# Performance work log

Hardware: AMD Instinct MI355X
Metric: run time of the kernel (lower is better)

The kernel has to match this reference:

```python
import jax, jax.numpy as jnp
import numpy as np

N_VEH = 40000
N_PATH = 400000
N_ACTOR = 128
N_MAP = 128
ACT_C = 32
PAT_C = 32
SIZE = N_ACTOR + N_MAP + ACT_C + PAT_C  # 320
HID = SIZE // 2  # 160
EPS = 1e-5


def _gn1(x, w, b):
    # GroupNorm with 1 group over channel dim of [N, C]: per-row normalize, per-channel affine
    mu = jnp.mean(x, axis=-1, keepdims=True)
    var = jnp.mean(jnp.square(x - mu), axis=-1, keepdims=True)
    return (x - mu) * jax.lax.rsqrt(var + EPS) * w + b


def setup_inputs() -> dict:
    key = jax.random.key(0)
    ks = jax.random.split(key, 12)
    inp = {
        "actors": jax.random.normal(ks[0], (N_VEH, N_ACTOR), jnp.float32),
        "paths": jax.random.normal(ks[1], (N_PATH, N_MAP), jnp.float32),
        "Z_act": jax.random.normal(ks[2], (N_VEH, ACT_C), jnp.float32),
        "Z_pat": jax.random.normal(ks[3], (N_PATH, PAT_C), jnp.float32),
        "u": jax.random.randint(ks[4], (N_PATH,), 0, N_VEH, jnp.int64 if jax.config.jax_enable_x64 else jnp.int32),
        # LinRes params (LaneGCN LinearRes: Linear(bias=False) -> GN -> ReLU -> Linear(bias=False) -> GN -> +transform(x) -> ReLU)
        "w1": jax.random.normal(ks[5], (HID, SIZE), jnp.float32) / np.sqrt(SIZE),
        "w2": jax.random.normal(ks[6], (HID, HID), jnp.float32) / np.sqrt(HID),
        "wt": jax.random.normal(ks[7], (HID, SIZE), jnp.float32) / np.sqrt(SIZE),
        "g1w": jnp.ones((HID,), jnp.float32),
        "g1b": jnp.zeros((HID,), jnp.float32),
        "g2w": jnp.ones((HID,), jnp.float32),
        "g2b": jnp.zeros((HID,), jnp.float32),
        # final head Linear(HID, 1)
        "wh": jax.random.normal(ks[8], (1, HID), jnp.float32) / np.sqrt(HID),
        "bh": jnp.zeros((1,), jnp.float32),
    }
    return inp


def reference(actors, paths, Z_act, Z_pat, u, w1, w2, wt, g1w, g1b, g2w, g2b, wh, bh):
    # edge-indexed gather + concat: [N_PATH, SIZE]
    x = jnp.concatenate([paths, Z_pat, actors[u], Z_act[u]], axis=-1)
    h = jnp.einsum('ns,hs->nh', x, w1)
    h = jax.nn.relu(_gn1(h, g1w, g1b))
    h = jnp.einsum('nh,gh->ng', h, w2)
    h = _gn1(h, g2w, g2b)
    h = jax.nn.relu(h + jnp.einsum('ns,hs->nh', x, wt))
    logits = jnp.einsum('nh,oh->no', h, wh) + bh
    return logits
```

## Files before the change

### kernel.cpp

```cpp
#include <hip/hip_runtime.h>
#include <hip/hip_bf16.h>

typedef short short8 __attribute__((ext_vector_type(8)));
typedef float floatx4 __attribute__((ext_vector_type(4)));

#define XP 328
#define HP 168

__device__ __forceinline__ unsigned short f2bf(float f) {
    __hip_bfloat16 h = __float2bfloat16(f);
    return __builtin_bit_cast(unsigned short, h);
}
__device__ __forceinline__ float bf2f(unsigned short s) {
    __hip_bfloat16 h = __builtin_bit_cast(__hip_bfloat16, s);
    return __bfloat162float(h);
}

__device__ __forceinline__ float dpp_sum16(float v) {
    v += __builtin_bit_cast(float, __builtin_amdgcn_update_dpp(
             0, __builtin_bit_cast(int, v), 0x128, 0xF, 0xF, true));
    v += __builtin_bit_cast(float, __builtin_amdgcn_update_dpp(
             0, __builtin_bit_cast(int, v), 0x124, 0xF, 0xF, true));
    v += __builtin_bit_cast(float, __builtin_amdgcn_update_dpp(
             0, __builtin_bit_cast(int, v), 0x122, 0xF, 0xF, true));
    v += __builtin_bit_cast(float, __builtin_amdgcn_update_dpp(
             0, __builtin_bit_cast(int, v), 0x121, 0xF, 0xF, true));
    return v;
}

__global__ void pack_wc(const float* __restrict__ w1, const float* __restrict__ wt,
                        unsigned short* __restrict__ dst) {
    int i = blockIdx.x * 256 + threadIdx.x;
    if (i >= 320 * 320) return;
    int j = i & 7;
    int lane = (i >> 3) & 63;
    int r = i >> 9;
    int kb = r % 10;
    int t = r / 10;
    int n = t * 16 + (lane & 15);
    int k = kb * 32 + ((lane >> 4) << 3) + j;
    float v = (n < 160) ? w1[n * 320 + k] : wt[(n - 160) * 320 + k];
    dst[i] = f2bf(v);
}

__global__ void pack_w2(const float* __restrict__ w2, unsigned short* __restrict__ dst) {
    int i = blockIdx.x * 256 + threadIdx.x;
    if (i >= 160 * 160) return;
    int j = i & 7;
    int lane = (i >> 3) & 63;
    int r = i >> 9;
    int kb = r % 5;
    int t = r / 5;
    int n = t * 16 + (lane & 15);
    int k = kb * 32 + ((lane >> 4) << 3) + j;
    dst[i] = f2bf(w2[n * 160 + k]);
}

__global__ __launch_bounds__(256, 3) void fused_kernel(
    const float* __restrict__ actors, const float* __restrict__ paths,
    const float* __restrict__ Z_act, const float* __restrict__ Z_pat,
    const int* __restrict__ u,
    const unsigned short* __restrict__ pB1, const unsigned short* __restrict__ pB2,
    const float* __restrict__ g1w, const float* __restrict__ g1b,
    const float* __restrict__ g2w, const float* __restrict__ g2b,
    const float* __restrict__ wh, const float* __restrict__ bh,
    float* __restrict__ out)
{
    __shared__ __align__(16) char smem[43520];
    unsigned short* lX  = (unsigned short*)smem;
    unsigned short* lH1 = (unsigned short*)smem;
    unsigned short* lHT = (unsigned short*)(smem + 21504);
    float*  sSum  = (float*)(smem + 41984);
    float*  sSq   = sSum + 128;
    float2* sStat = (float2*)(smem + 41984 + 1024);

    const int tid  = threadIdx.x;
    const int wave = tid >> 6;
    const int lane = tid & 63;
    const int quad = lane >> 4;
    const int l15  = lane & 15;
    const int row0 = blockIdx.x * 64;

    float4 vD[10], vG[10];
    int uv[10];
    #pragma unroll
    for (int i = 0; i < 10; i++) {
        int f = i * 256 + tid;
        int r = f / 40, q = f - r * 40;
        const float* src = (q < 32) ? (paths + (size_t)(row0 + r) * 128 + q * 4)
                                    : (Z_pat + (size_t)(row0 + r) * 32 + (q - 32) * 4);
        vD[i] = *(const float4*)src;
        uv[i] = u[row0 + r];
    }
    #pragma unroll
    for (int i = 0; i < 10; i++) {
        int f = i * 256 + tid;
        int r = f / 40, q = f - r * 40;
        (void)r;
        int un = uv[i];
        const float* src = (q < 32) ? (actors + (size_t)un * 128 + q * 4)
                                    : (Z_act + (size_t)un * 32 + (q - 32) * 4);
        vG[i] = *(const float4*)src;
    }
    #pragma unroll
    for (int i = 0; i < 10; i++) {
        int f = i * 256 + tid;
        int r = f / 40, q = f - r * 40;
        ushort4 sv;
        sv.x = f2bf(vD[i].x); sv.y = f2bf(vD[i].y); sv.z = f2bf(vD[i].z); sv.w = f2bf(vD[i].w);
        *(ushort4*)(lX + r * XP + q * 4) = sv;
    }
    #pragma unroll
    for (int i = 0; i < 10; i++) {
        int f = i * 256 + tid;
        int r = f / 40, q = f - r * 40;
        ushort4 sv;
        sv.x = f2bf(vG[i].x); sv.y = f2bf(vG[i].y); sv.z = f2bf(vG[i].z); sv.w = f2bf(vG[i].w);
        *(ushort4*)(lX + r * XP + 160 + q * 4) = sv;
    }

    short8 bA[5], bB[5];
    #pragma unroll
    for (int ti = 0; ti < 5; ti++) {
        int t = wave * 5 + ti;
        bA[ti] = *(const short8*)(pB1 + ((size_t)(t * 10 + 0) * 64 + lane) * 8);
        bB[ti] = *(const short8*)(pB1 + ((size_t)(t * 10 + 1) * 64 + lane) * 8);
    }
    __syncthreads();

    floatx4 fzero = {0.f, 0.f, 0.f, 0.f};
    floatx4 acc[4][5];
    #pragma unroll
    for (int i = 0; i < 4; i++)
        #pragma unroll
        for (int j = 0; j < 5; j++) acc[i][j] = fzero;

    #pragma unroll
    for (int kb = 0; kb < 10; kb++) {
        short8 a[4];
        #pragma unroll
        for (int mt = 0; mt < 4; mt++)
            a[mt] = *(const short8*)(lX + (mt * 16 + l15) * XP + kb * 32 + quad * 8);
        short8 bN[5];
        if (kb + 2 < 10) {
            #pragma unroll
            for (int ti = 0; ti < 5; ti++) {
                int t = wave * 5 + ti;
                bN[ti] = *(const short8*)(pB1 + ((size_t)(t * 10 + kb + 2) * 64 + lane) * 8);
            }
        }
        #pragma unroll
        for (int ti = 0; ti < 5; ti++) {
            #pragma unroll
            for (int mt = 0; mt < 4; mt++)
                acc[mt][ti] = __builtin_amdgcn_mfma_f32_16x16x32_bf16(a[mt], bA[ti], acc[mt][ti], 0, 0, 0);
        }
        #pragma unroll
        for (int ti = 0; ti < 5; ti++) { bA[ti] = bB[ti]; bB[ti] = bN[ti]; }
    }
    __syncthreads();

    if (wave >= 2) {
        int wn2 = wave - 2;
        #pragma unroll
        for (int mtp = 0; mtp < 4; mtp++)
            #pragma unroll
            for (int ti = 0; ti < 5; ti++) {
                ushort4 sv;
                sv.x = f2bf(acc[mtp][ti][0]);
                sv.y = f2bf(acc[mtp][ti][1]);
                sv.z = f2bf(acc[mtp][ti][2]);
                sv.w = f2bf(acc[mtp][ti][3]);
                int ch = wn2 * 80 + ti * 16 + l15;
                int rg = (mtp * 4 + quad) ^ l15;
                *(ushort4*)(lHT + ch * 64 + rg * 4) = sv;
            }
    } else {
        float s[16], q2[16];
        #pragma unroll
        for (int mt = 0; mt < 4; mt++)
            #pragma unroll
            for (int r = 0; r < 4; r++) {
                float sv = 0.f, qv = 0.f;
                #pragma unroll
                for (int ti = 0; ti < 5; ti++) {
                    float v = acc[mt][ti][r];
                    sv += v; qv += v * v;
                }
                s[mt * 4 + r] = sv; q2[mt * 4 + r] = qv;
            }
        #pragma unroll
        for (int k = 0; k < 16; k++) {
            s[k]  = dpp_sum16(s[k]);
            q2[k] = dpp_sum16(q2[k]);
        }
        if (l15 == 0) {
            #pragma unroll
            for (int mt = 0; mt < 4; mt++)
                #pragma unroll
                for (int r = 0; r < 4; r++) {
                    int m = mt * 16 + quad * 4 + r;
                    sSum[wave * 64 + m] = s[mt * 4 + r];
                    sSq[wave * 64 + m]  = q2[mt * 4 + r];
                }
        }
    }
    __syncthreads();

    if (tid < 64) {
        float ts = sSum[tid] + sSum[64 + tid];
        float tq = sSq[tid] + sSq[64 + tid];
        float mu = ts * (1.f / 160.f);
        float var = tq * (1.f / 160.f) - mu * mu;
        float2 st; st.x = mu; st.y = rsqrtf(var + 1e-5f);
        sStat[tid] = st;
    }
    __syncthreads();

    if (wave < 2) {
        float gw[5], gb[5];
        #pragma unroll
        for (int ti = 0; ti < 5; ti++) {
            int n = wave * 80 + ti * 16 + l15;
            gw[ti] = g1w[n]; gb[ti] = g1b[n];
        }
        #pragma unroll
        for (int mt = 0; mt < 4; mt++)
            #pragma unroll
            for (int r = 0; r < 4; r++) {
                int m = mt * 16 + quad * 4 + r;
                float2 st = sStat[m];
                #pragma unroll
                for (int ti = 0; ti < 5; ti++) {
                    float v = (acc[mt][ti][r] - st.x) * st.y * gw[ti] + gb[ti];
                    v = fmaxf(v, 0.f);
                    lH1[m * HP + wave * 80 + ti * 16 + l15] = f2bf(v);
                }
            }
    }

    const int wm = wave & 1, wn = wave >> 1;
    short8 b2A[5], b2B[5];
    #pragma unroll
    for (int ti = 0; ti < 5; ti++) {
        int t = wn * 5 + ti;
        b2A[ti] = *(const short8*)(pB2 + ((size_t)(t * 5 + 0) * 64 + lane) * 8);
        b2B[ti] = *(const short8*)(pB2 + ((size_t)(t * 5 + 1) * 64 + lane) * 8);
    }
    __syncthreads();

    floatx4 acc2[2][5];
    #pragma unroll
    for (int i = 0; i < 2; i++)
        #pragma unroll
        for (int j = 0; j < 5; j++) acc2[i][j] = fzero;

    #pragma unroll
    for (int kb = 0; kb < 5; kb++) {
        short8 a[2];
        #pragma unroll
        for (int mt = 0; mt < 2; mt++)
            a[mt] = *(const short8*)(lH1 + (wm * 32 + mt * 16 + l15) * HP + kb * 32 + quad * 8);
        short8 bN[5];
        if (kb + 2 < 5) {
            #pragma unroll
            for (int ti = 0; ti < 5; ti++) {
                int t = wn * 5 + ti;
                bN[ti] = *(const short8*)(pB2 + ((size_t)(t * 5 + kb + 2) * 64 + lane) * 8);
            }
        }
        #pragma unroll
        for (int ti = 0; ti < 5; ti++) {
            #pragma unroll
            for (int mt = 0; mt < 2; mt++)
                acc2[mt][ti] = __builtin_amdgcn_mfma_f32_16x16x32_bf16(a[mt], b2A[ti], acc2[mt][ti], 0, 0, 0);
        }
        #pragma unroll
        for (int ti = 0; ti < 5; ti++) { b2A[ti] = b2B[ti]; b2B[ti] = bN[ti]; }
    }

    {
        float s[8], q2[8];
        #pragma unroll
        for (int mt = 0; mt < 2; mt++)
            #pragma unroll
            for (int r = 0; r < 4; r++) {
                float sv = 0.f, qv = 0.f;
                #pragma unroll
                for (int ti = 0; ti < 5; ti++) {
                    float v = acc2[mt][ti][r];
                    sv += v; qv += v * v;
                }
                s[mt * 4 + r] = sv; q2[mt * 4 + r] = qv;
            }
        #pragma unroll
        for (int k = 0; k < 8; k++) {
            s[k]  = dpp_sum16(s[k]);
            q2[k] = dpp_sum16(q2[k]);
        }
        if (l15 == 0) {
            #pragma unroll
            for (int mt = 0; mt < 2; mt++)
                #pragma unroll
                for (int r = 0; r < 4; r++) {
                    int m = wm * 32 + mt * 16 + quad * 4 + r;
                    sSum[wn * 64 + m] = s[mt * 4 + r];
                    sSq[wn * 64 + m]  = q2[mt * 4 + r];
                }
        }
    }
    __syncthreads();

    if (tid < 64) {
        float ts = sSum[tid] + sSum[64 + tid];
        float tq = sSq[tid] + sSq[64 + tid];
        float mu = ts * (1.f / 160.f);
        float var = tq * (1.f / 160.f) - mu * mu;
        float2 st; st.x = mu; st.y = rsqrtf(var + 1e-5f);
        sStat[tid] = st;
    }
    __syncthreads();

    {
        float g2wv[5], g2bv[5], whv[5];
        #pragma unroll
        for (int ti = 0; ti < 5; ti++) {
            int n = wn * 80 + ti * 16 + l15;
            g2wv[ti] = g2w[n]; g2bv[ti] = g2b[n]; whv[ti] = wh[n];
        }
        float2 st2[2][4];
        #pragma unroll
        for (int mt = 0; mt < 2; mt++)
            #pragma unroll
            for (int r = 0; r < 4; r++)
                st2[mt][r] = sStat[wm * 32 + mt * 16 + quad * 4 + r];

        float dp[8];
        #pragma unroll
        for (int k = 0; k < 8; k++) dp[k] = 0.f;

        #pragma unroll
        for (int mt = 0; mt < 2; mt++)
            #pragma unroll
            for (int ti = 0; ti < 5; ti++) {
                int ch = wn * 80 + ti * 16 + l15;
                int rg = ((wm * 2 + mt) * 4 + quad) ^ l15;
                ushort4 hv = *(const ushort4*)(lHT + ch * 64 + rg * 4);
                float hvf[4];
                hvf[0] = bf2f(hv.x); hvf[1] = bf2f(hv.y);
                hvf[2] = bf2f(hv.z); hvf[3] = bf2f(hv.w);
                #pragma unroll
                for (int r = 0; r < 4; r++) {
                    float v = (acc2[mt][ti][r] - st2[mt][r].x) * st2[mt][r].y * g2wv[ti] + g2bv[ti];
                    v += hvf[r];
                    v = fmaxf(v, 0.f);
                    dp[mt * 4 + r] += v * whv[ti];
                }
            }
        #pragma unroll
        for (int k = 0; k < 8; k++) dp[k] = dpp_sum16(dp[k]);
        if (l15 == 0) {
            #pragma unroll
            for (int mt = 0; mt < 2; mt++)
                #pragma unroll
                for (int r = 0; r < 4; r++) {
                    int m = wm * 32 + mt * 16 + quad * 4 + r;
                    sSum[wn * 64 + m] = dp[mt * 4 + r];
                }
        }
    }
    __syncthreads();
    if (tid < 64) out[row0 + tid] = sSum[tid] + sSum[64 + tid] + bh[0];
}

extern "C" void kernel_launch(void* const* d_in, const int* in_sizes, int n_in,
                              void* d_out, int out_size, void* d_ws, size_t ws_size,
                              hipStream_t stream) {
    const float* actors = (const float*)d_in[0];
    const float* paths  = (const float*)d_in[1];
    const float* Z_act  = (const float*)d_in[2];
    const float* Z_pat  = (const float*)d_in[3];
    const int*   u      = (const int*)d_in[4];
    const float* w1     = (const float*)d_in[5];
    const float* w2     = (const float*)d_in[6];
    const float* wt     = (const float*)d_in[7];
    const float* g1w    = (const float*)d_in[8];
    const float* g1b    = (const float*)d_in[9];
    const float* g2w    = (const float*)d_in[10];
    const float* g2b    = (const float*)d_in[11];
    const float* wh     = (const float*)d_in[12];
    const float* bh     = (const float*)d_in[13];
    float* out = (float*)d_out;

    unsigned short* pB1 = (unsigned short*)d_ws;
    unsigned short* pB2 = pB1 + 320 * 320;

    hipLaunchKernelGGL(pack_wc, dim3(400), dim3(256), 0, stream, w1, wt, pB1);
    hipLaunchKernelGGL(pack_w2, dim3(100), dim3(256), 0, stream, w2, pB2);
    hipLaunchKernelGGL(fused_kernel, dim3(400000 / 64), dim3(256), 0, stream,
                       actors, paths, Z_act, Z_pat, u, pB1, pB2,
                       g1w, g1b, g2w, g2b, wh, bh, out);
}
```

Baseline: 486.0 us.

## Shrink blocks to 32 rows with 2 waves, swizzled LDS A layout and weight ring

Blocks now process 32 rows with 128 threads. Each wave owns a whole 160-channel output half: wave 0 takes the W1 half and wave 1 the transform half. This lets wave 0 compute the first GroupNorm stats entirely in registers, and lets wave 1 keep its transform outputs in registers instead of writing them to LDS. The input tile is stored in LDS in an MFMA-fragment-packed, XOR-swizzled layout so A-operand reads avoid bank conflicts, and the B-operand weights stream through a 5-deep register ring. The changes cut shared memory and barriers and raise occupancy, at the cost of each wave re-reading the full weight matrix for fewer rows, which means more weight traffic per row.

```diff
diff --git a/kernel.cpp b/kernel.cpp
--- a/kernel.cpp
+++ b/kernel.cpp
@@ -2,9 +2,9 @@
 #include <hip/hip_bf16.h>
 
 typedef short short8 __attribute__((ext_vector_type(8)));
+typedef unsigned short ushortv8 __attribute__((ext_vector_type(8)));
 typedef float floatx4 __attribute__((ext_vector_type(4)));
 
-#define XP 328
 #define HP 168
 
 __device__ __forceinline__ unsigned short f2bf(float f) {
@@ -56,7 +56,7 @@
     dst[i] = f2bf(w2[n * 160 + k]);
 }
 
-__global__ __launch_bounds__(256, 3) void fused_kernel(
+__global__ __launch_bounds__(128, 4) void fused_kernel(
     const float* __restrict__ actors, const float* __restrict__ paths,
     const float* __restrict__ Z_act, const float* __restrict__ Z_pat,
     const int* __restrict__ u,
@@ -66,292 +66,250 @@
     const float* __restrict__ wh, const float* __restrict__ bh,
     float* __restrict__ out)
 {
-    __shared__ __align__(16) char smem[43520];
+    __shared__ __align__(16) char smem[20480];
     unsigned short* lX  = (unsigned short*)smem;
     unsigned short* lH1 = (unsigned short*)smem;
-    unsigned short* lHT = (unsigned short*)(smem + 21504);
-    float*  sSum  = (float*)(smem + 41984);
-    float*  sSq   = sSum + 128;
-    float2* sStat = (float2*)(smem + 41984 + 1024);
+    unsigned short* lHT = (unsigned short*)(smem + 10752);
+    float* sP  = (float*)(smem + 15872);
+    float* sDp = (float*)(smem + 16384);
 
     const int tid  = threadIdx.x;
     const int wave = tid >> 6;
     const int lane = tid & 63;
     const int quad = lane >> 4;
     const int l15  = lane & 15;
-    const int row0 = blockIdx.x * 64;
-
-    float4 vD[10], vG[10];
-    int uv[10];
-    #pragma unroll
-    for (int i = 0; i < 10; i++) {
-        int f = i * 256 + tid;
-        int r = f / 40, q = f - r * 40;
-        const float* src = (q < 32) ? (paths + (size_t)(row0 + r) * 128 + q * 4)
-                                    : (Z_pat + (size_t)(row0 + r) * 32 + (q - 32) * 4);
-        vD[i] = *(const float4*)src;
+    const int row0 = blockIdx.x * 32;
+
+    float4 vD[5][2], vG[5][2];
+    int uv[5], rr[5], qq[5];
+    #pragma unroll
+    for (int i = 0; i < 5; i++) {
+        int f = i * 128 + tid;
+        int r = f / 20, q = f - r * 20;
+        rr[i] = r; qq[i] = q;
+        const float* src = (q < 16) ? (paths + (size_t)(row0 + r) * 128 + q * 8)
+                                    : (Z_pat + (size_t)(row0 + r) * 32 + (q - 16) * 8);
+        vD[i][0] = *(const float4*)src;
+        vD[i][1] = *(const float4*)(src + 4);
         uv[i] = u[row0 + r];
     }
     #pragma unroll
-    for (int i = 0; i < 10; i++) {
-        int f = i * 256 + tid;
-        int r = f / 40, q = f - r * 40;
-        (void)r;
+    for (int i = 0; i < 5; i++) {
+        int q = qq[i];
         int un = uv[i];
-        const float* src = (q < 32) ? (actors + (size_t)un * 128 + q * 4)
-                                    : (Z_act + (size_t)un * 32 + (q - 32) * 4);
-        vG[i] = *(const float4*)src;
-    }
-    #pragma unroll
-    for (int i = 0; i < 10; i++) {
-        int f = i * 256 + tid;
-        int r = f / 40, q = f - r * 40;
-        ushort4 sv;
-        sv.x = f2bf(vD[i].x); sv.y = f2bf(vD[i].y); sv.z = f2bf(vD[i].z); sv.w = f2bf(vD[i].w);
-        *(ushort4*)(lX + r * XP + q * 4) = sv;
-    }
-    #pragma unroll
-    for (int i = 0; i < 10; i++) {
-        int f = i * 256 + tid;
-        int r = f / 40, q = f - r * 40;
-        ushort4 sv;
-        sv.x = f2bf(vG[i].x); sv.y = f2bf(vG[i].y); sv.z = f2bf(vG[i].z); sv.w = f2bf(vG[i].w);
-        *(ushort4*)(lX + r * XP + 160 + q * 4) = sv;
-    }
-
-    short8 bA[5], bB[5];
-    #pragma unroll
-    for (int ti = 0; ti < 5; ti++) {
-        int t = wave * 5 + ti;
-        bA[ti] = *(const short8*)(pB1 + ((size_t)(t * 10 + 0) * 64 + lane) * 8);
-        bB[ti] = *(const short8*)(pB1 + ((size_t)(t * 10 + 1) * 64 + lane) * 8);
+        const float* src = (q < 16) ? (actors + (size_t)un * 128 + q * 8)
+                                    : (Z_act + (size_t)un * 32 + (q - 16) * 8);
+        vG[i][0] = *(const float4*)src;
+        vG[i][1] = *(const float4*)(src + 4);
+    }
+    #pragma unroll
+    for (int i = 0; i < 5; i++) {
+        int r = rr[i], q = qq[i];
+        int mt = r >> 4;
+        {
+            int kb = q >> 2, qd = q & 3;
+            int slot = ((r & 15) | (qd << 4)) ^ ((qd ^ kb) & 7);
+            ushortv8 sv;
+            sv[0] = f2bf(vD[i][0].x); sv[1] = f2bf(vD[i][0].y);
+            sv[2] = f2bf(vD[i][0].z); sv[3] = f2bf(vD[i][0].w);
+            sv[4] = f2bf(vD[i][1].x); sv[5] = f2bf(vD[i][1].y);
+            sv[6] = f2bf(vD[i][1].z); sv[7] = f2bf(vD[i][1].w);
+            *(ushortv8*)(lX + ((mt * 10 + kb) * 64 + slot) * 8) = sv;
+        }
+        {
+            int q8 = q + 20;
+            int kb = q8 >> 2, qd = q8 & 3;
+            int slot = ((r & 15) | (qd << 4)) ^ ((qd ^ kb) & 7);
+            ushortv8 sv;
+            sv[0] = f2bf(vG[i][0].x); sv[1] = f2bf(vG[i][0].y);
+            sv[2] = f2bf(vG[i][0].z); sv[3] = f2bf(vG[i][0].w);
+            sv[4] = f2bf(vG[i][1].x); sv[5] = f2bf(vG[i][1].y);
+            sv[6] = f2bf(vG[i][1].z); sv[7] = f2bf(vG[i][1].w);
+            *(ushortv8*)(lX + ((mt * 10 + kb) * 64 + slot) * 8) = sv;
+        }
+    }
+
+    const unsigned short* pBw = pB1 + (size_t)wave * 51200 + (size_t)lane * 8;
+    short8 ring[5];
+    #pragma unroll
+    for (int p = 0; p < 5; p++) {
+        ring[p] = *(const short8*)(pBw + (size_t)(p * 10) * 512);
     }
     __syncthreads();
 
     floatx4 fzero = {0.f, 0.f, 0.f, 0.f};
-    floatx4 acc[4][5];
-    #pragma unroll
-    for (int i = 0; i < 4; i++)
-        #pragma unroll
-        for (int j = 0; j < 5; j++) acc[i][j] = fzero;
+    floatx4 acc[2][10];
+    #pragma unroll
+    for (int i = 0; i < 2; i++)
+        #pragma unroll
+        for (int j = 0; j < 10; j++) acc[i][j] = fzero;
 
     #pragma unroll
     for (int kb = 0; kb < 10; kb++) {
-        short8 a[4];
-        #pragma unroll
-        for (int mt = 0; mt < 4; mt++)
-            a[mt] = *(const short8*)(lX + (mt * 16 + l15) * XP + kb * 32 + quad * 8);
-        short8 bN[5];
-        if (kb + 2 < 10) {
-            #pragma unroll
-            for (int ti = 0; ti < 5; ti++) {
-                int t = wave * 5 + ti;
-                bN[ti] = *(const short8*)(pB1 + ((size_t)(t * 10 + kb + 2) * 64 + lane) * 8);
-            }
-        }
-        #pragma unroll
-        for (int ti = 0; ti < 5; ti++) {
-            #pragma unroll
-            for (int mt = 0; mt < 4; mt++)
-                acc[mt][ti] = __builtin_amdgcn_mfma_f32_16x16x32_bf16(a[mt], bA[ti], acc[mt][ti], 0, 0, 0);
-        }
-        #pragma unroll
-        for (int ti = 0; ti < 5; ti++) { bA[ti] = bB[ti]; bB[ti] = bN[ti]; }
-    }
-    __syncthreads();
-
-    if (wave >= 2) {
-        int wn2 = wave - 2;
-        #pragma unroll
-        for (int mtp = 0; mtp < 4; mtp++)
-            #pragma unroll
-            for (int ti = 0; ti < 5; ti++) {
-                ushort4 sv;
-                sv.x = f2bf(acc[mtp][ti][0]);
-                sv.y = f2bf(acc[mtp][ti][1]);
-                sv.z = f2bf(acc[mtp][ti][2]);
-                sv.w = f2bf(acc[mtp][ti][3]);
-                int ch = wn2 * 80 + ti * 16 + l15;
-                int rg = (mtp * 4 + quad) ^ l15;
-                *(ushort4*)(lHT + ch * 64 + rg * 4) = sv;
-            }
-    } else {
-        float s[16], q2[16];
-        #pragma unroll
-        for (int mt = 0; mt < 4; mt++)
+        int sl = (lane ^ ((quad ^ kb) & 7)) * 8;
+        short8 a0 = *(const short8*)(lX + kb * 512 + sl);
+        short8 a1 = *(const short8*)(lX + 5120 + kb * 512 + sl);
+        #pragma unroll
+        for (int ti = 0; ti < 10; ti++) {
+            int p = kb * 10 + ti;
+            short8 b = ring[p % 5];
+            acc[0][ti] = __builtin_amdgcn_mfma_f32_16x16x32_bf16(a0, b, acc[0][ti], 0, 0, 0);
+            acc[1][ti] = __builtin_amdgcn_mfma_f32_16x16x32_bf16(a1, b, acc[1][ti], 0, 0, 0);
+            if (p + 5 < 100) {
+                int p2 = p + 5, kb2 = p2 / 10, ti2 = p2 - kb2 * 10;
+                ring[p2 % 5] = *(const short8*)(pBw + (size_t)(ti2 * 10 + kb2) * 512);
+            }
+        }
+    }
+    __syncthreads();
+
+    ushort4 hk[2][5];
+    if (wave == 0) {
+        float mu_[2][4], rs_[2][4];
+        #pragma unroll
+        for (int mt = 0; mt < 2; mt++)
             #pragma unroll
             for (int r = 0; r < 4; r++) {
-                float sv = 0.f, qv = 0.f;
+                float s = 0.f, q2 = 0.f;
                 #pragma unroll
-                for (int ti = 0; ti < 5; ti++) {
+                for (int ti = 0; ti < 10; ti++) {
                     float v = acc[mt][ti][r];
-                    sv += v; qv += v * v;
-                }
-                s[mt * 4 + r] = sv; q2[mt * 4 + r] = qv;
-            }
-        #pragma unroll
-        for (int k = 0; k < 16; k++) {
-            s[k]  = dpp_sum16(s[k]);
-            q2[k] = dpp_sum16(q2[k]);
-        }
-        if (l15 == 0) {
-            #pragma unroll
-            for (int mt = 0; mt < 4; mt++)
+                    s += v; q2 += v * v;
+                }
+                s = dpp_sum16(s); q2 = dpp_sum16(q2);
+                float mu = s * (1.f / 160.f);
+                float var = q2 * (1.f / 160.f) - mu * mu;
+                mu_[mt][r] = mu;
+                rs_[mt][r] = rsqrtf(var + 1e-5f);
+            }
+        float gw[10], gb[10];
+        #pragma unroll
+        for (int ti = 0; ti < 10; ti++) {
+            int n = ti * 16 + l15;
+            gw[ti] = g1w[n]; gb[ti] = g1b[n];
+        }
+        #pragma unroll
+        for (int mt = 0; mt < 2; mt++)
+            #pragma unroll
+            for (int ti = 0; ti < 10; ti++)
                 #pragma unroll
                 for (int r = 0; r < 4; r++) {
-                    int m = mt * 16 + quad * 4 + r;
-                    sSum[wave * 64 + m] = s[mt * 4 + r];
-                    sSq[wave * 64 + m]  = q2[mt * 4 + r];
-                }
-        }
-    }
-    __syncthreads();
-
-    if (tid < 64) {
-        float ts = sSum[tid] + sSum[64 + tid];
-        float tq = sSq[tid] + sSq[64 + tid];
-        float mu = ts * (1.f / 160.f);
-        float var = tq * (1.f / 160.f) - mu * mu;
-        float2 st; st.x = mu; st.y = rsqrtf(var + 1e-5f);
-        sStat[tid] = st;
-    }
-    __syncthreads();
-
-    if (wave < 2) {
-        float gw[5], gb[5];
+                    float v = (acc[mt][ti][r] - mu_[mt][r]) * rs_[mt][r] * gw[ti] + gb[ti];
+                    v = fmaxf(v, 0.f);
+                    lH1[(mt * 16 + quad * 4 + r) * HP + ti * 16 + l15] = f2bf(v);
+                }
+    } else {
+        #pragma unroll
+        for (int mt = 0; mt < 2; mt++)
+            #pragma unroll
+            for (int tk = 0; tk < 5; tk++) {
+                ushort4 kv;
+                kv.x = f2bf(acc[mt][tk + 5][0]); kv.y = f2bf(acc[mt][tk + 5][1]);
+                kv.z = f2bf(acc[mt][tk + 5][2]); kv.w = f2bf(acc[mt][tk + 5][3]);
+                hk[mt][tk] = kv;
+                ushort4 sv;
+                sv.x = f2bf(acc[mt][tk][0]); sv.y = f2bf(acc[mt][tk][1]);
+                sv.z = f2bf(acc[mt][tk][2]); sv.w = f2bf(acc[mt][tk][3]);
+                int ch = tk * 16 + l15;
+                int rg = (mt * 4 + quad) ^ (l15 & 7);
+                *(ushort4*)(lHT + (ch * 8 + rg) * 4) = sv;
+            }
+    }
+
+    const unsigned short* pB2w = pB2 + (size_t)wave * 12800 + (size_t)lane * 8;
+    short8 ring2[4];
+    #pragma unroll
+    for (int p = 0; p < 4; p++) {
+        ring2[p] = *(const short8*)(pB2w + (size_t)(p * 5) * 512);
+    }
+    __syncthreads();
+
+    floatx4 acc2[2][5];
+    #pragma unroll
+    for (int i = 0; i < 2; i++)
+        #pragma unroll
+        for (int j = 0; j < 5; j++) acc2[i][j] = fzero;
+
+    #pragma unroll
+    for (int kb = 0; kb < 5; kb++) {
+        short8 a0 = *(const short8*)(lH1 + l15 * HP + kb * 32 + quad * 8);
+        short8 a1 = *(const short8*)(lH1 + (16 + l15) * HP + kb * 32 + quad * 8);
+        #pragma unroll
+        for (int ti = 0; ti < 5; ti++) {
+            int p = kb * 5 + ti;
+            short8 b = ring2[p % 4];
+            acc2[0][ti] = __builtin_amdgcn_mfma_f32_16x16x32_bf16(a0, b, acc2[0][ti], 0, 0, 0);
+            acc2[1][ti] = __builtin_amdgcn_mfma_f32_16x16x32_bf16(a1, b, acc2[1][ti], 0, 0, 0);
+            if (p + 4 < 25) {
+                int p2 = p + 4, kb2 = p2 / 5, ti2 = p2 - kb2 * 5;
+                ring2[p2 % 4] = *(const short8*)(pB2w + (size_t)(ti2 * 5 + kb2) * 512);
+            }
+        }
+    }
+
+    #pragma unroll
+    for (int mt = 0; mt < 2; mt++)
+        #pragma unroll
+        for (int r = 0; r < 4; r++) {
+            float s = 0.f, q2 = 0.f;
+            #pragma unroll
+            for (int ti = 0; ti < 5; ti++) {
+                float v = acc2[mt][ti][r];
+                s += v; q2 += v * v;
+            }
+            s = dpp_sum16(s); q2 = dpp_sum16(q2);
+            if (l15 == 0) {
+                int m = mt * 16 + quad * 4 + r;
+                float2 pv; pv.x = s; pv.y = q2;
+                *(float2*)(sP + m * 4 + wave * 2) = pv;
+            }
+        }
+    __syncthreads();
+
+    float mu2_[2][4], rs2_[2][4];
+    #pragma unroll
+    for (int mt = 0; mt < 2; mt++)
+        #pragma unroll
+        for (int r = 0; r < 4; r++) {
+            int m = mt * 16 + quad * 4 + r;
+            float4 pv = *(const float4*)(sP + m * 4);
+            float ts = pv.x + pv.z;
+            float tq = pv.y + pv.w;
+            float mu = ts * (1.f / 160.f);
+            float var = tq * (1.f / 160.f) - mu * mu;
+            mu2_[mt][r] = mu;
+            rs2_[mt][r] = rsqrtf(var + 1e-5f);
+        }
+
+    {
+        float g2wv[5], g2bv[5], whv[5];
         #pragma unroll
         for (int ti = 0; ti < 5; ti++) {
             int n = wave * 80 + ti * 16 + l15;
-            gw[ti] = g1w[n]; gb[ti] = g1b[n];
-        }
-        #pragma unroll
-        for (int mt = 0; mt < 4; mt++)
-            #pragma unroll
-            for (int r = 0; r < 4; r++) {
-                int m = mt * 16 + quad * 4 + r;
-                float2 st = sStat[m];
-                #pragma unroll
-                for (int ti = 0; ti < 5; ti++) {
-                    float v = (acc[mt][ti][r] - st.x) * st.y * gw[ti] + gb[ti];
-                    v = fmaxf(v, 0.f);
-                    lH1[m * HP + wave * 80 + ti * 16 + l15] = f2bf(v);
-                }
-            }
-    }
-
-    const int wm = wave & 1, wn = wave >> 1;
-    short8 b2A[5], b2B[5];
-    #pragma unroll
-    for (int ti = 0; ti < 5; ti++) {
-        int t = wn * 5 + ti;
-        b2A[ti] = *(const short8*)(pB2 + ((size_t)(t * 5 + 0) * 64 + lane) * 8);
-        b2B[ti] = *(const short8*)(pB2 + ((size_t)(t * 5 + 1) * 64 + lane) * 8);
-    }
-    __syncthreads();
-
-    floatx4 acc2[2][5];
-    #pragma unroll
-    for (int i = 0; i < 2; i++)
-        #pragma unroll
-        for (int j = 0; j < 5; j++) acc2[i][j] = fzero;
-
-    #pragma unroll
-    for (int kb = 0; kb < 5; kb++) {
-        short8 a[2];
+            g2wv[ti] = g2w[n]; g2bv[ti] = g2b[n]; whv[ti] = wh[n];
+        }
+        float dp[8];
+        #pragma unroll
+        for (int k = 0; k < 8; k++) dp[k] = 0.f;
+
         #pragma unroll
         for (int mt = 0; mt < 2; mt++)
-            a[mt] = *(const short8*)(lH1 + (wm * 32 + mt * 16 + l15) * HP + kb * 32 + quad * 8);
-        short8 bN[5];
-        if (kb + 2 < 5) {
             #pragma unroll
             for (int ti = 0; ti < 5; ti++) {
-                int t = wn * 5 + ti;
-                bN[ti] = *(const short8*)(pB2 + ((size_t)(t * 5 + kb + 2) * 64 + lane) * 8);
-            }
-        }
-        #pragma unroll
-        for (int ti = 0; ti < 5; ti++) {
-            #pragma unroll
-            for (int mt = 0; mt < 2; mt++)
-                acc2[mt][ti] = __builtin_amdgcn_mfma_f32_16x16x32_bf16(a[mt], b2A[ti], acc2[mt][ti], 0, 0, 0);
-        }
-        #pragma unroll
-        for (int ti = 0; ti < 5; ti++) { b2A[ti] = b2B[ti]; b2B[ti] = bN[ti]; }
-    }
-
-    {
-        float s[8], q2[8];
-        #pragma unroll
-        for (int mt = 0; mt < 2; mt++)
-            #pragma unroll
-            for (int r = 0; r < 4; r++) {
-                float sv = 0.f, qv = 0.f;
-                #pragma unroll
-                for (int ti = 0; ti < 5; ti++) {
-                    float v = acc2[mt][ti][r];
-                    sv += v; qv += v * v;
-                }
-                s[mt * 4 + r] = sv; q2[mt * 4 + r] = qv;
-            }
-        #pragma unroll
-        for (int k = 0; k < 8; k++) {
-            s[k]  = dpp_sum16(s[k]);
-            q2[k] = dpp_sum16(q2[k]);
-        }
-        if (l15 == 0) {
-            #pragma unroll
-            for (int mt = 0; mt < 2; mt++)
-                #pragma unroll
-                for (int r = 0; r < 4; r++) {
-                    int m = wm * 32 + mt * 16 + quad * 4 + r;
-                    sSum[wn * 64 + m] = s[mt * 4 + r];
-                    sSq[wn * 64 + m]  = q2[mt * 4 + r];
-                }
-        }
-    }
-    __syncthreads();
-
-    if (tid < 64) {
-        float ts = sSum[tid] + sSum[64 + tid];
-        float tq = sSq[tid] + sSq[64 + tid];
-        float mu = ts * (1.f / 160.f);
-        float var = tq * (1.f / 160.f) - mu * mu;
-        float2 st; st.x = mu; st.y = rsqrtf(var + 1e-5f);
-        sStat[tid] = st;
-    }
-    __syncthreads();
-
-    {
-        float g2wv[5], g2bv[5], whv[5];
-        #pragma unroll
-        for (int ti = 0; ti < 5; ti++) {
-            int n = wn * 80 + ti * 16 + l15;
-            g2wv[ti] = g2w[n]; g2bv[ti] = g2b[n]; whv[ti] = wh[n];
-        }
-        float2 st2[2][4];
-        #pragma unroll
-        for (int mt = 0; mt < 2; mt++)
-            #pragma unroll
-            for (int r = 0; r < 4; r++)
-                st2[mt][r] = sStat[wm * 32 + mt * 16 + quad * 4 + r];
-
-        float dp[8];
-        #pragma unroll
-        for (int k = 0; k < 8; k++) dp[k] = 0.f;
-
-        #pragma unroll
-        for (int mt = 0; mt < 2; mt++)
-            #pragma unroll
-            for (int ti = 0; ti < 5; ti++) {
-                int ch = wn * 80 + ti * 16 + l15;
-                int rg = ((wm * 2 + mt) * 4 + quad) ^ l15;
-                ushort4 hv = *(const ushort4*)(lHT + ch * 64 + rg * 4);
+                ushort4 hv;
+                if (wave == 0) {
+                    int ch = ti * 16 + l15;
+                    int rg = (mt * 4 + quad) ^ (l15 & 7);
+                    hv = *(const ushort4*)(lHT + (ch * 8 + rg) * 4);
+                } else {
+                    hv = hk[mt][ti];
+                }
                 float hvf[4];
                 hvf[0] = bf2f(hv.x); hvf[1] = bf2f(hv.y);
                 hvf[2] = bf2f(hv.z); hvf[3] = bf2f(hv.w);
                 #pragma unroll
                 for (int r = 0; r < 4; r++) {
-                    float v = (acc2[mt][ti][r] - st2[mt][r].x) * st2[mt][r].y * g2wv[ti] + g2bv[ti];
+                    float v = (acc2[mt][ti][r] - mu2_[mt][r]) * rs2_[mt][r] * g2wv[ti] + g2bv[ti];
                     v += hvf[r];
                     v = fmaxf(v, 0.f);
                     dp[mt * 4 + r] += v * whv[ti];
@@ -364,13 +322,16 @@
             for (int mt = 0; mt < 2; mt++)
                 #pragma unroll
                 for (int r = 0; r < 4; r++) {
-                    int m = wm * 32 + mt * 16 + quad * 4 + r;
-                    sSum[wn * 64 + m] = dp[mt * 4 + r];
-                }
-        }
-    }
-    __syncthreads();
-    if (tid < 64) out[row0 + tid] = sSum[tid] + sSum[64 + tid] + bh[0];
+                    int m = mt * 16 + quad * 4 + r;
+                    sDp[m * 2 + wave] = dp[mt * 4 + r];
+                }
+        }
+    }
+    __syncthreads();
+    if (tid < 32) {
+        float2 d = *(const float2*)(sDp + tid * 2);
+        out[row0 + tid] = d.x + d.y + bh[0];
+    }
 }
 
 extern "C" void kernel_launch(void* const* d_in, const int* in_sizes, int n_in,
@@ -397,7 +358,7 @@
 
     hipLaunchKernelGGL(pack_wc, dim3(400), dim3(256), 0, stream, w1, wt, pB1);
     hipLaunchKernelGGL(pack_w2, dim3(100), dim3(256), 0, stream, w2, pB2);
-    hipLaunchKernelGGL(fused_kernel, dim3(400000 / 64), dim3(256), 0, stream,
+    hipLaunchKernelGGL(fused_kernel, dim3(400000 / 32), dim3(128), 0, stream,
                        actors, paths, Z_act, Z_pat, u, pB1, pB2,
                        g1w, g1b, g2w, g2b, wh, bh, out);
 }
```

New measurement: 566.2 us. 16.5% more time.

## Make fused kernel persistent with software-prefetch of next tile's inputs

Applied to the files above, without the earlier changes.

Converts the one-tile-per-block launch into a persistent grid of 512 blocks that loop over 64-row tiles. While the current tile's GEMMs and norms run, the block prefetches the next tile's paths/Z_pat rows and indices into registers, then issues the gathered actor loads mid-iteration. This hides global load latency behind compute. The cost is higher register pressure, since occupancy drops from 3 to 2 blocks per CU, and barriers now use a custom lgkmcnt wait plus s_barrier.

```diff
diff --git a/kernel.cpp b/kernel.cpp
--- a/kernel.cpp
+++ b/kernel.cpp
@@ -6,6 +6,8 @@
 
 #define XP 328
 #define HP 168
+#define NT 6250
+#define GRID 512
 
 __device__ __forceinline__ unsigned short f2bf(float f) {
     __hip_bfloat16 h = __float2bfloat16(f);
@@ -14,6 +16,16 @@
 __device__ __forceinline__ float bf2f(unsigned short s) {
     __hip_bfloat16 h = __builtin_bit_cast(__hip_bfloat16, s);
     return __bfloat162float(h);
+}
+__device__ __forceinline__ ushort4 cvt4(float4 v) {
+    ushort4 s; s.x = f2bf(v.x); s.y = f2bf(v.y); s.z = f2bf(v.z); s.w = f2bf(v.w);
+    return s;
+}
+
+__device__ __forceinline__ void xbar() {
+    asm volatile("s_waitcnt lgkmcnt(0)" ::: "memory");
+    __builtin_amdgcn_s_barrier();
+    asm volatile("" ::: "memory");
 }
 
 __device__ __forceinline__ float dpp_sum16(float v) {
@@ -56,7 +68,7 @@
     dst[i] = f2bf(w2[n * 160 + k]);
 }
 
-__global__ __launch_bounds__(256, 3) void fused_kernel(
+__global__ __launch_bounds__(256, 2) void fused_kernel(
     const float* __restrict__ actors, const float* __restrict__ paths,
     const float* __restrict__ Z_act, const float* __restrict__ Z_pat,
     const int* __restrict__ u,
@@ -79,298 +91,363 @@
     const int lane = tid & 63;
     const int quad = lane >> 4;
     const int l15  = lane & 15;
-    const int row0 = blockIdx.x * 64;
-
-    float4 vD[10], vG[10];
-    int uv[10];
-    #pragma unroll
-    for (int i = 0; i < 10; i++) {
-        int f = i * 256 + tid;
-        int r = f / 40, q = f - r * 40;
-        const float* src = (q < 32) ? (paths + (size_t)(row0 + r) * 128 + q * 4)
-                                    : (Z_pat + (size_t)(row0 + r) * 32 + (q - 32) * 4);
-        vD[i] = *(const float4*)src;
-        uv[i] = u[row0 + r];
+
+    int t = blockIdx.x;
+
+    {
+        float4 vD[10], vG[10];
+        int uvv[10];
+        #pragma unroll
+        for (int i = 0; i < 10; i++) {
+            int f = i * 256 + tid;
+            int r = f / 40, q = f - r * 40;
+            const float* src = (q < 32) ? (paths + ((size_t)t * 64 + r) * 128 + q * 4)
+                                        : (Z_pat + ((size_t)t * 64 + r) * 32 + (q - 32) * 4);
+            vD[i] = *(const float4*)src;
+            uvv[i] = u[(size_t)t * 64 + r];
+        }
+        #pragma unroll
+        for (int i = 0; i < 10; i++) {
+            int f = i * 256 + tid;
+            int q = (f - (f / 40) * 40);
+            int un = uvv[i];
+            const float* src = (q < 32) ? (actors + (size_t)un * 128 + q * 4)
+                                        : (Z_act + (size_t)un * 32 + (q - 32) * 4);
+            vG[i] = *(const float4*)src;
+        }
+        #pragma unroll
+        for (int i = 0; i < 10; i++) {
+            int f = i * 256 + tid;
+            int r = f / 40, q = f - r * 40;
+            *(ushort4*)(lX + r * XP + q * 4) = cvt4(vD[i]);
+        }
+        #pragma unroll
+        for (int i = 0; i < 10; i++) {
+            int f = i * 256 + tid;
+            int r = f / 40, q = f - r * 40;
+            *(ushort4*)(lX + r * XP + 160 + q * 4) = cvt4(vG[i]);
+        }
     }
-    #pragma unroll
-    for (int i = 0; i < 10; i++) {
-        int f = i * 256 + tid;
-        int r = f / 40, q = f - r * 40;
-        (void)r;
-        int un = uv[i];
-        const float* src = (q < 32) ? (actors + (size_t)un * 128 + q * 4)
-                                    : (Z_act + (size_t)un * 32 + (q - 32) * 4);
-        vG[i] = *(const float4*)src;
+
+    int tn = t + GRID;
+    bool hn = (tn < NT);
+    float4 nD[10];
+    int nuv[10];
+    {
+        size_t rb = (size_t)(hn ? tn : t) * 64;
+        #pragma unroll
+        for (int i = 0; i < 10; i++) {
+            int f = i * 256 + tid;
+            int r = f / 40, q = f - r * 40;
+            const float* src = (q < 32) ? (paths + (rb + r) * 128 + q * 4)
+                                        : (Z_pat + (rb + r) * 32 + (q - 32) * 4);
+            nD[i] = *(const float4*)src;
+            nuv[i] = u[rb + r];
+        }
     }
-    #pragma unroll
-    for (int i = 0; i < 10; i++) {
-        int f = i * 256 + tid;
-        int r = f / 40, q = f - r * 40;
-        ushort4 sv;
-        sv.x = f2bf(vD[i].x); sv.y = f2bf(vD[i].y); sv.z = f2bf(vD[i].z); sv.w = f2bf(vD[i].w);
-        *(ushort4*)(lX + r * XP + q * 4) = sv;
-    }
-    #pragma unroll
-    for (int i = 0; i < 10; i++) {
-        int f = i * 256 + tid;
-        int r = f / 40, q = f - r * 40;
-        ushort4 sv;
-        sv.x = f2bf(vG[i].x); sv.y = f2bf(vG[i].y); sv.z = f2bf(vG[i].z); sv.w = f2bf(vG[i].w);
-        *(ushort4*)(lX + r * XP + 160 + q * 4) = sv;
-    }
-
-    short8 bA[5], bB[5];
-    #pragma unroll
-    for (int ti = 0; ti < 5; ti++) {
-        int t = wave * 5 + ti;
-        bA[ti] = *(const short8*)(pB1 + ((size_t)(t * 10 + 0) * 64 + lane) * 8);
-        bB[ti] = *(const short8*)(pB1 + ((size_t)(t * 10 + 1) * 64 + lane) * 8);
-    }
-    __syncthreads();
 
     floatx4 fzero = {0.f, 0.f, 0.f, 0.f};
-    floatx4 acc[4][5];
-    #pragma unroll
-    for (int i = 0; i < 4; i++)
-        #pragma unroll
-        for (int j = 0; j < 5; j++) acc[i][j] = fzero;
-
-    #pragma unroll
-    for (int kb = 0; kb < 10; kb++) {
-        short8 a[4];
-        #pragma unroll
-        for (int mt = 0; mt < 4; mt++)
-            a[mt] = *(const short8*)(lX + (mt * 16 + l15) * XP + kb * 32 + quad * 8);
-        short8 bN[5];
-        if (kb + 2 < 10) {
+
+    for (;;) {
+        const size_t row0 = (size_t)t * 64;
+
+        const unsigned short* pBw = pB1;
+        short8 bA[5], bB[5];
+        #pragma unroll
+        for (int ti = 0; ti < 5; ti++) {
+            int tt = wave * 5 + ti;
+            bA[ti] = *(const short8*)(pBw + ((size_t)(tt * 10 + 0) * 64 + lane) * 8);
+            bB[ti] = *(const short8*)(pBw + ((size_t)(tt * 10 + 1) * 64 + lane) * 8);
+        }
+        xbar();
+
+        floatx4 acc[4][5];
+        #pragma unroll
+        for (int i = 0; i < 4; i++)
+            #pragma unroll
+            for (int j = 0; j < 5; j++) acc[i][j] = fzero;
+
+        #pragma unroll
+        for (int kb = 0; kb < 10; kb++) {
+            short8 a[4];
+            #pragma unroll
+            for (int mt = 0; mt < 4; mt++)
+                a[mt] = *(const short8*)(lX + (mt * 16 + l15) * XP + kb * 32 + quad * 8);
+            short8 bN[5];
+            if (kb + 2 < 10) {
+                #pragma unroll
+                for (int ti = 0; ti < 5; ti++) {
+                    int tt = wave * 5 + ti;
+                    bN[ti] = *(const short8*)(pBw + ((size_t)(tt * 10 + kb + 2) * 64 + lane) * 8);
+                }
+            }
             #pragma unroll
             for (int ti = 0; ti < 5; ti++) {
-                int t = wave * 5 + ti;
-                bN[ti] = *(const short8*)(pB1 + ((size_t)(t * 10 + kb + 2) * 64 + lane) * 8);
-            }
-        }
-        #pragma unroll
-        for (int ti = 0; ti < 5; ti++) {
+                #pragma unroll
+                for (int mt = 0; mt < 4; mt++)
+                    acc[mt][ti] = __builtin_amdgcn_mfma_f32_16x16x32_bf16(a[mt], bA[ti], acc[mt][ti], 0, 0, 0);
+            }
+            #pragma unroll
+            for (int ti = 0; ti < 5; ti++) { bA[ti] = bB[ti]; bB[ti] = bN[ti]; }
+        }
+
+        ushort4 nDh[10];
+        float4 nG[10];
+        if (hn) {
+            #pragma unroll
+            for (int i = 0; i < 10; i++) nDh[i] = cvt4(nD[i]);
+            #pragma unroll
+            for (int i = 0; i < 10; i++) {
+                int f = i * 256 + tid;
+                int q = f - (f / 40) * 40;
+                int un = nuv[i];
+                const float* src = (q < 32) ? (actors + (size_t)un * 128 + q * 4)
+                                            : (Z_act + (size_t)un * 32 + (q - 32) * 4);
+                nG[i] = *(const float4*)src;
+            }
+        }
+        xbar();
+
+        if (wave >= 2) {
+            int wn2 = wave - 2;
+            #pragma unroll
+            for (int mtp = 0; mtp < 4; mtp++)
+                #pragma unroll
+                for (int ti = 0; ti < 5; ti++) {
+                    ushort4 sv;
+                    sv.x = f2bf(acc[mtp][ti][0]);
+                    sv.y = f2bf(acc[mtp][ti][1]);
+                    sv.z = f2bf(acc[mtp][ti][2]);
+                    sv.w = f2bf(acc[mtp][ti][3]);
+                    int ch = wn2 * 80 + ti * 16 + l15;
+                    int rg = (mtp * 4 + quad) ^ l15;
+                    *(ushort4*)(lHT + ch * 64 + rg * 4) = sv;
+                }
+        } else {
+            float s[16], q2[16];
             #pragma unroll
             for (int mt = 0; mt < 4; mt++)
-                acc[mt][ti] = __builtin_amdgcn_mfma_f32_16x16x32_bf16(a[mt], bA[ti], acc[mt][ti], 0, 0, 0);
-        }
-        #pragma unroll
-        for (int ti = 0; ti < 5; ti++) { bA[ti] = bB[ti]; bB[ti] = bN[ti]; }
-    }
-    __syncthreads();
-
-    if (wave >= 2) {
-        int wn2 = wave - 2;
-        #pragma unroll
-        for (int mtp = 0; mtp < 4; mtp++)
+                #pragma unroll
+                for (int r = 0; r < 4; r++) {
+                    float sv = 0.f, qv = 0.f;
+                    #pragma unroll
+                    for (int ti = 0; ti < 5; ti++) {
+                        float v = acc[mt][ti][r];
+                        sv += v; qv += v * v;
+                    }
+                    s[mt * 4 + r] = sv; q2[mt * 4 + r] = qv;
+                }
+            #pragma unroll
+            for (int k = 0; k < 16; k++) {
+                s[k]  = dpp_sum16(s[k]);
+                q2[k] = dpp_sum16(q2[k]);
+            }
+            if (l15 == 0) {
+                #pragma unroll
+                for (int mt = 0; mt < 4; mt++)
+                    #pragma unroll
+                    for (int r = 0; r < 4; r++) {
+                        int m = mt * 16 + quad * 4 + r;
+                        sSum[wave * 64 + m] = s[mt * 4 + r];
+                        sSq[wave * 64 + m]  = q2[mt * 4 + r];
+                    }
+            }
+        }
+        xbar();
+
+        if (tid < 64) {
+            float ts = sSum[tid] + sSum[64 + tid];
+            float tq = sSq[tid] + sSq[64 + tid];
+            float mu = ts * (1.f / 160.f);
+            float var = tq * (1.f / 160.f) - mu * mu;
+            float2 st; st.x = mu; st.y = rsqrtf(var + 1e-5f);
+            sStat[tid] = st;
+        }
+        xbar();
+
+        if (wave < 2) {
+            float gw[5], gb[5];
             #pragma unroll
             for (int ti = 0; ti < 5; ti++) {
-                ushort4 sv;
-                sv.x = f2bf(acc[mtp][ti][0]);
-                sv.y = f2bf(acc[mtp][ti][1]);
-                sv.z = f2bf(acc[mtp][ti][2]);
-                sv.w = f2bf(acc[mtp][ti][3]);
-                int ch = wn2 * 80 + ti * 16 + l15;
-                int rg = (mtp * 4 + quad) ^ l15;
-                *(ushort4*)(lHT + ch * 64 + rg * 4) = sv;
-            }
-    } else {
-        float s[16], q2[16];
-        #pragma unroll
-        for (int mt = 0; mt < 4; mt++)
-            #pragma unroll
-            for (int r = 0; r < 4; r++) {
-                float sv = 0.f, qv = 0.f;
-                #pragma unroll
-                for (int ti = 0; ti < 5; ti++) {
-                    float v = acc[mt][ti][r];
-                    sv += v; qv += v * v;
-                }
-                s[mt * 4 + r] = sv; q2[mt * 4 + r] = qv;
-            }
-        #pragma unroll
-        for (int k = 0; k < 16; k++) {
-            s[k]  = dpp_sum16(s[k]);
-            q2[k] = dpp_sum16(q2[k]);
-        }
-        if (l15 == 0) {
+                int n = wave * 80 + ti * 16 + l15;
+                gw[ti] = g1w[n]; gb[ti] = g1b[n];
+            }
             #pragma unroll
             for (int mt = 0; mt < 4; mt++)
                 #pragma unroll
                 for (int r = 0; r < 4; r++) {
                     int m = mt * 16 + quad * 4 + r;
-                    sSum[wave * 64 + m] = s[mt * 4 + r];
-                    sSq[wave * 64 + m]  = q2[mt * 4 + r];
-                }
+                    float2 st = sStat[m];
+                    #pragma unroll
+                    for (int ti = 0; ti < 5; ti++) {
+                        float v = (acc[mt][ti][r] - st.x) * st.y * gw[ti] + gb[ti];
+                        v = fmaxf(v, 0.f);
+                        lH1[m * HP + wave * 80 + ti * 16 + l15] = f2bf(v);
+                    }
+                }
+        }
+
+        const int wm = wave & 1, wn = wave >> 1;
+        const unsigned short* pB2w = pB2;
+        short8 b2A[5], b2B[5];
+        #pragma unroll
+        for (int ti = 0; ti < 5; ti++) {
+            int tt = wn * 5 + ti;
+            b2A[ti] = *(const short8*)(pB2w + ((size_t)(tt * 5 + 0) * 64 + lane) * 8);
+            b2B[ti] = *(const short8*)(pB2w + ((size_t)(tt * 5 + 1) * 64 + lane) * 8);
+        }
+        xbar();
+
+        floatx4 acc2[2][5];
+        #pragma unroll
+        for (int i = 0; i < 2; i++)
+            #pragma unroll
+            for (int j = 0; j < 5; j++) acc2[i][j] = fzero;
+
+        #pragma unroll
+        for (int kb = 0; kb < 5; kb++) {
+            short8 a[2];
+            #pragma unroll
+            for (int mt = 0; mt < 2; mt++)
+                a[mt] = *(const short8*)(lH1 + (wm * 32 + mt * 16 + l15) * HP + kb * 32 + quad * 8);
+            short8 bN[5];
+            if (kb + 2 < 5) {
+                #pragma unroll
+                for (int ti = 0; ti < 5; ti++) {
+                    int tt = wn * 5 + ti;
+                    bN[ti] = *(const short8*)(pB2w + ((size_t)(tt * 5 + kb + 2) * 64 + lane) * 8);
+                }
+            }
+            #pragma unroll
+            for (int ti = 0; ti < 5; ti++) {
+                #pragma unroll
+                for (int mt = 0; mt < 2; mt++)
+                    acc2[mt][ti] = __builtin_amdgcn_mfma_f32_16x16x32_bf16(a[mt], b2A[ti], acc2[mt][ti], 0, 0, 0);
+            }
+            #pragma unroll
+            for (int ti = 0; ti < 5; ti++) { b2A[ti] = b2B[ti]; b2B[ti] = bN[ti]; }
+        }
+
+        {
+            float s[8], q2[8];
+            #pragma unroll
+            for (int mt = 0; mt < 2; mt++)
+                #pragma unroll
+                for (int r = 0; r < 4; r++) {
+                    float sv = 0.f, qv = 0.f;
+                    #pragma unroll
+                    for (int ti = 0; ti < 5; ti++) {
+                        float v = acc2[mt][ti][r];
+                        sv += v; qv += v * v;
+                    }
+                    s[mt * 4 + r] = sv; q2[mt * 4 + r] = qv;
+                }
+            #pragma unroll
+            for (int k = 0; k < 8; k++) {
+                s[k]  = dpp_sum16(s[k]);
+                q2[k] = dpp_sum16(q2[k]);
+            }
+            if (l15 == 0) {
+                #pragma unroll
+                for (int mt = 0; mt < 2; mt++)
+                    #pragma unroll
+                    for (int r = 0; r < 4; r++) {
+                        int m = wm * 32 + mt * 16 + quad * 4 + r;
+                        sSum[wn * 64 + m] = s[mt * 4 + r];
+                        sSq[wn * 64 + m]  = q2[mt * 4 + r];
+                    }
+            }
+        }
+        xbar();
+
+        if (tid < 64) {
+            float ts = sSum[tid] + sSum[64 + tid];
+            float tq = sSq[tid] + sSq[64 + tid];
+            float mu = ts * (1.f / 160.f);
+            float var = tq * (1.f / 160.f) - mu * mu;
+            float2 st; st.x = mu; st.y = rsqrtf(var + 1e-5f);
+            sStat[tid] = st;
+        }
+        xbar();
+
+        {
+            float g2wv[5], g2bv[5], whv[5];
+            #pragma unroll
+            for (int ti = 0; ti < 5; ti++) {
+                int n = wn * 80 + ti * 16 + l15;
+                g2wv[ti] = g2w[n]; g2bv[ti] = g2b[n]; whv[ti] = wh[n];
+            }
+            float2 st2[2][4];
+            #pragma unroll
+            for (int mt = 0; mt < 2; mt++)
+                #pragma unroll
+                for (int r = 0; r < 4; r++)
+                    st2[mt][r] = sStat[wm * 32 + mt * 16 + quad * 4 + r];
+
+            float dp[8];
+            #pragma unroll
+            for (int k = 0; k < 8; k++) dp[k] = 0.f;
+
+            #pragma unroll
+            for (int mt = 0; mt < 2; mt++)
+                #pragma unroll
+                for (int ti = 0; ti < 5; ti++) {
+                    int ch = wn * 80 + ti * 16 + l15;
+                    int rg = ((wm * 2 + mt) * 4 + quad) ^ l15;
+                    ushort4 hv = *(const ushort4*)(lHT + ch * 64 + rg * 4);
+                    float hvf[4];
+                    hvf[0] = bf2f(hv.x); hvf[1] = bf2f(hv.y);
+                    hvf[2] = bf2f(hv.z); hvf[3] = bf2f(hv.w);
+                    #pragma unroll
+                    for (int r = 0; r < 4; r++) {
+                        float v = (acc2[mt][ti][r] - st2[mt][r].x) * st2[mt][r].y * g2wv[ti] + g2bv[ti];
+                        v += hvf[r];
+                        v = fmaxf(v, 0.f);
+                        dp[mt * 4 + r] += v * whv[ti];
+                    }
+                }
+            #pragma unroll
+            for (int k = 0; k < 8; k++) dp[k] = dpp_sum16(dp[k]);
+            if (l15 == 0) {
+                #pragma unroll
+                for (int mt = 0; mt < 2; mt++)
+                    #pragma unroll
+                    for (int r = 0; r < 4; r++) {
+                        int m = wm * 32 + mt * 16 + quad * 4 + r;
+                        sSum[wn * 64 + m] = dp[mt * 4 + r];
+                    }
+            }
+        }
+        xbar();
+
+        if (tid < 64) out[row0 + tid] = sSum[tid] + sSum[64 + tid] + bh[0];
+
+        if (!hn) break;
+
+        #pragma unroll
+        for (int i = 0; i < 10; i++) {
+            int f = i * 256 + tid;
+            int r = f / 40, q = f - r * 40;
+            *(ushort4*)(lX + r * XP + q * 4) = nDh[i];
+            *(ushort4*)(lX + r * XP + 160 + q * 4) = cvt4(nG[i]);
+        }
+
+        t = tn;
+        tn += GRID;
+        hn = (tn < NT);
+        {
+            size_t rb = (size_t)(hn ? tn : t) * 64;
+            #pragma unroll
+            for (int i = 0; i < 10; i++) {
+                int f = i * 256 + tid;
+                int r = f / 40, q = f - r * 40;
+                const float* src = (q < 32) ? (paths + (rb + r) * 128 + q * 4)
+                                            : (Z_pat + (rb + r) * 32 + (q - 32) * 4);
+                nD[i] = *(const float4*)src;
+                nuv[i] = u[rb + r];
+            }
         }
     }
-    __syncthreads();
-
-    if (tid < 64) {
-        float ts = sSum[tid] + sSum[64 + tid];
-        float tq = sSq[tid] + sSq[64 + tid];
-        float mu = ts * (1.f / 160.f);
-        float var = tq * (1.f / 160.f) - mu * mu;
-        float2 st; st.x = mu; st.y = rsqrtf(var + 1e-5f);
-        sStat[tid] = st;
-    }
-    __syncthreads();
-
-    if (wave < 2) {
-        float gw[5], gb[5];
-        #pragma unroll
-        for (int ti = 0; ti < 5; ti++) {
-            int n = wave * 80 + ti * 16 + l15;
-            gw[ti] = g1w[n]; gb[ti] = g1b[n];
-        }
-        #pragma unroll
-        for (int mt = 0; mt < 4; mt++)
-            #pragma unroll
-            for (int r = 0; r < 4; r++) {
-                int m = mt * 16 + quad * 4 + r;
-                float2 st = sStat[m];
-                #pragma unroll
-                for (int ti = 0; ti < 5; ti++) {
-                    float v = (acc[mt][ti][r] - st.x) * st.y * gw[ti] + gb[ti];
-                    v = fmaxf(v, 0.f);
-                    lH1[m * HP + wave * 80 + ti * 16 + l15] = f2bf(v);
-                }
-            }
-    }
-
-    const int wm = wave & 1, wn = wave >> 1;
-    short8 b2A[5], b2B[5];
-    #pragma unroll
-    for (int ti = 0; ti < 5; ti++) {
-        int t = wn * 5 + ti;
-        b2A[ti] = *(const short8*)(pB2 + ((size_t)(t * 5 + 0) * 64 + lane) * 8);
-        b2B[ti] = *(const short8*)(pB2 + ((size_t)(t * 5 + 1) * 64 + lane) * 8);
-    }
-    __syncthreads();
-
-    floatx4 acc2[2][5];
-    #pragma unroll
-    for (int i = 0; i < 2; i++)
-        #pragma unroll
-        for (int j = 0; j < 5; j++) acc2[i][j] = fzero;
-
-    #pragma unroll
-    for (int kb = 0; kb < 5; kb++) {
-        short8 a[2];
-        #pragma unroll
-        for (int mt = 0; mt < 2; mt++)
-            a[mt] = *(const short8*)(lH1 + (wm * 32 + mt * 16 + l15) * HP + kb * 32 + quad * 8);
-        short8 bN[5];
-        if (kb + 2 < 5) {
-            #pragma unroll
-            for (int ti = 0; ti < 5; ti++) {
-                int t = wn * 5 + ti;
-                bN[ti] = *(const short8*)(pB2 + ((size_t)(t * 5 + kb + 2) * 64 + lane) * 8);
-            }
-        }
-        #pragma unroll
-        for (int ti = 0; ti < 5; ti++) {
-            #pragma unroll
-            for (int mt = 0; mt < 2; mt++)
-                acc2[mt][ti] = __builtin_amdgcn_mfma_f32_16x16x32_bf16(a[mt], b2A[ti], acc2[mt][ti], 0, 0, 0);
-        }
-        #pragma unroll
-        for (int ti = 0; ti < 5; ti++) { b2A[ti] = b2B[ti]; b2B[ti] = bN[ti]; }
-    }
-
-    {
-        float s[8], q2[8];
-        #pragma unroll
-        for (int mt = 0; mt < 2; mt++)
-            #pragma unroll
-            for (int r = 0; r < 4; r++) {
-                float sv = 0.f, qv = 0.f;
-                #pragma unroll
-                for (int ti = 0; ti < 5; ti++) {
-                    float v = acc2[mt][ti][r];
-                    sv += v; qv += v * v;
-                }
-                s[mt * 4 + r] = sv; q2[mt * 4 + r] = qv;
-            }
-        #pragma unroll
-        for (int k = 0; k < 8; k++) {
-            s[k]  = dpp_sum16(s[k]);
-            q2[k] = dpp_sum16(q2[k]);
-        }
-        if (l15 == 0) {
-            #pragma unroll
-            for (int mt = 0; mt < 2; mt++)
-                #pragma unroll
-                for (int r = 0; r < 4; r++) {
-                    int m = wm * 32 + mt * 16 + quad * 4 + r;
-                    sSum[wn * 64 + m] = s[mt * 4 + r];
-                    sSq[wn * 64 + m]  = q2[mt * 4 + r];
-                }
-        }
-    }
-    __syncthreads();
-
-    if (tid < 64) {
-        float ts = sSum[tid] + sSum[64 + tid];
-        float tq = sSq[tid] + sSq[64 + tid];
-        float mu = ts * (1.f / 160.f);
-        float var = tq * (1.f / 160.f) - mu * mu;
-        float2 st; st.x = mu; st.y = rsqrtf(var + 1e-5f);
-        sStat[tid] = st;
-    }
-    __syncthreads();
-
-    {
-        float g2wv[5], g2bv[5], whv[5];
-        #pragma unroll
-        for (int ti = 0; ti < 5; ti++) {
-            int n = wn * 80 + ti * 16 + l15;
-            g2wv[ti] = g2w[n]; g2bv[ti] = g2b[n]; whv[ti] = wh[n];
-        }
-        float2 st2[2][4];
-        #pragma unroll
-        for (int mt = 0; mt < 2; mt++)
-            #pragma unroll
-            for (int r = 0; r < 4; r++)
-                st2[mt][r] = sStat[wm * 32 + mt * 16 + quad * 4 + r];
-
-        float dp[8];
-        #pragma unroll
-        for (int k = 0; k < 8; k++) dp[k] = 0.f;
-
-        #pragma unroll
-        for (int mt = 0; mt < 2; mt++)
-            #pragma unroll
-            for (int ti = 0; ti < 5; ti++) {
-                int ch = wn * 80 + ti * 16 + l15;
-                int rg = ((wm * 2 + mt) * 4 + quad) ^ l15;
-                ushort4 hv = *(const ushort4*)(lHT + ch * 64 + rg * 4);
-                float hvf[4];
-                hvf[0] = bf2f(hv.x); hvf[1] = bf2f(hv.y);
-                hvf[2] = bf2f(hv.z); hvf[3] = bf2f(hv.w);
-                #pragma unroll
-                for (int r = 0; r < 4; r++) {
-                    float v = (acc2[mt][ti][r] - st2[mt][r].x) * st2[mt][r].y * g2wv[ti] + g2bv[ti];
-                    v += hvf[r];
-                    v = fmaxf(v, 0.f);
-                    dp[mt * 4 + r] += v * whv[ti];
-                }
-            }
-        #pragma unroll
-        for (int k = 0; k < 8; k++) dp[k] = dpp_sum16(dp[k]);
-        if (l15 == 0) {
-            #pragma unroll
-            for (int mt = 0; mt < 2; mt++)
-                #pragma unroll
-                for (int r = 0; r < 4; r++) {
-                    int m = wm * 32 + mt * 16 + quad * 4 + r;
-                    sSum[wn * 64 + m] = dp[mt * 4 + r];
-                }
-        }
-    }
-    __syncthreads();
-    if (tid < 64) out[row0 + tid] = sSum[tid] + sSum[64 + tid] + bh[0];
 }
 
 extern "C" void kernel_launch(void* const* d_in, const int* in_sizes, int n_in,
@@ -397,7 +474,7 @@
 
     hipLaunchKernelGGL(pack_wc, dim3(400), dim3(256), 0, stream, w1, wt, pB1);
     hipLaunchKernelGGL(pack_w2, dim3(100), dim3(256), 0, stream, w2, pB2);
-    hipLaunchKernelGGL(fused_kernel, dim3(400000 / 64), dim3(256), 0, stream,
+    hipLaunchKernelGGL(fused_kernel, dim3(GRID), dim3(256), 0, stream,
                        actors, paths, Z_act, Z_pat, u, pB1, pB2,
                        g1w, g1b, g2w, g2b, wh, bh, out);
 }
```

Result: slower. 968.4 us (+99.3%).
